# Kernel tuning notes

Hardware: AMD Instinct MI355X
Metric: run time of the kernel (lower is better)

## Reference

```python
import jax, jax.numpy as jnp
import numpy as np

H, D = 4, 64          # n_heads, feats_per_head (hidden_size = H*D = 256)
NEG_SLOPE = 0.2       # DGL GATv2Conv default negative_slope

N_GT, N_UBS, N_AG = 100000, 20000, 20000
E_SEEN, E_NEAR = 320000, 160000
F_GT, F_UBS, F_AG = 8, 8, 16
HID = H * D


def _linear_params(key, fan_in, fan_out):
    kw, kb = jax.random.split(key)
    s = 1.0 / np.sqrt(fan_in)
    W = jax.random.uniform(kw, (fan_in, fan_out), jnp.float32, -s, s)
    b = jax.random.uniform(kb, (fan_out,), jnp.float32, -s, s)
    return W, b


def setup_inputs() -> dict:
    key = jax.random.key(0)
    ks = jax.random.split(key, 16)
    inp = {
        'x_gt': jax.random.normal(ks[0], (N_GT, F_GT), jnp.float32),
        'x_ubs': jax.random.normal(ks[1], (N_UBS, F_UBS), jnp.float32),
        'x_agent': jax.random.normal(ks[2], (N_AG, F_AG), jnp.float32),
        'seen_src': jax.random.randint(ks[3], (E_SEEN,), 0, N_GT, jnp.int32),
        'seen_dst': jax.random.randint(ks[4], (E_SEEN,), 0, N_AG, jnp.int32),
        'near_src': jax.random.randint(ks[5], (E_NEAR,), 0, N_UBS, jnp.int32),
        'near_dst': jax.random.randint(ks[6], (E_NEAR,), 0, N_AG, jnp.int32),
    }
    # GATv2Conv 'seen': (gt -> agent)
    inp['Ws_seen'], inp['bs_seen'] = _linear_params(ks[7], F_GT, HID)
    inp['Wd_seen'], inp['bd_seen'] = _linear_params(ks[8], F_AG, HID)
    inp['attn_seen'] = jax.random.normal(ks[9], (H, D), jnp.float32) * 0.1
    inp['Wr_seen'], inp['br_seen'] = _linear_params(ks[10], F_AG, HID)
    # GATv2Conv 'near': (ubs -> agent)
    inp['Ws_near'], inp['bs_near'] = _linear_params(ks[11], F_UBS, HID)
    inp['Wd_near'], inp['bd_near'] = _linear_params(ks[12], F_AG, HID)
    inp['attn_near'] = jax.random.normal(ks[13], (H, D), jnp.float32) * 0.1
    inp['Wr_near'], inp['br_near'] = _linear_params(ks[14], F_AG, HID)
    # aggregation MLP: Linear(2*HID, HID) + ReLU
    inp['W_aggr'], inp['b_aggr'] = _linear_params(ks[15], 2 * HID, HID)
    return inp


def _gatv2(h_src, h_dst, src, dst, Ws, bs, Wd, bd, attn, Wr, br, n_dst):
    # DGL GATv2Conv, bipartite, residual=True, allow_zero_in_degree, ReLU activation
    fs = (h_src @ Ws + bs).reshape(-1, H, D)   # [Ns,H,D]
    fd = (h_dst @ Wd + bd).reshape(-1, H, D)   # [Nd,H,D]
    e = jax.nn.leaky_relu(fs[src] + fd[dst], NEG_SLOPE)     # [E,H,D]
    scores = jnp.einsum('ehd,hd->eh', e, attn)              # [E,H]
    # edge softmax over incoming edges of each dst node
    m = jax.ops.segment_max(scores, dst, num_segments=n_dst)
    m = jnp.where(jnp.isfinite(m), m, 0.0)                  # zero-in-degree guard
    ex = jnp.exp(scores - m[dst])
    denom = jax.ops.segment_sum(ex, dst, num_segments=n_dst)
    alpha = ex / denom[dst]                                 # [E,H]
    rst = jax.ops.segment_sum(alpha[:, :, None] * fs[src], dst, num_segments=n_dst)
    rst = rst + (h_dst @ Wr + br).reshape(-1, H, D)         # residual
    return jax.nn.relu(rst).reshape(n_dst, H * D)


def reference(x_gt, x_ubs, x_agent, seen_src, seen_dst, near_src, near_dst,
              Ws_seen, bs_seen, Wd_seen, bd_seen, attn_seen, Wr_seen, br_seen,
              Ws_near, bs_near, Wd_near, bd_near, attn_near, Wr_near, br_near,
              W_aggr, b_aggr):
    n_ag = x_agent.shape[0]
    x1 = _gatv2(x_gt, x_agent, seen_src, seen_dst,
                Ws_seen, bs_seen, Wd_seen, bd_seen, attn_seen, Wr_seen, br_seen, n_ag)
    x2 = _gatv2(x_ubs, x_agent, near_src, near_dst,
                Ws_near, bs_near, Wd_near, bd_near, attn_near, Wr_near, br_near, n_ag)
    x_out = jnp.concatenate((x1, x2), axis=1)               # [N_ag, 2*HID]
    return jax.nn.relu(x_out @ W_aggr + b_aggr)             # [N_ag, HID]
```

## Files before the change

kernel.cpp:

```cpp
#include <hip/hip_runtime.h>
#include <math.h>

#define NEG 0.2f
#define CAP 48

typedef short bf16x8 __attribute__((ext_vector_type(8)));
typedef float f32x4  __attribute__((ext_vector_type(4)));
typedef float f32x2  __attribute__((ext_vector_type(2)));

static __device__ __forceinline__ f32x2 pkfma(f32x2 a, f32x2 b, f32x2 c) {
    return __builtin_elementwise_fma(a, b, c);
}
static __device__ __forceinline__ f32x2 splat2(float x) { return (f32x2){x, x}; }

static __device__ __forceinline__ unsigned short f2bf(float f) {
    unsigned int x = __float_as_uint(f);
    unsigned int r = (x + 0x7FFFu + ((x >> 16) & 1u)) >> 16;
    return (unsigned short)r;
}
static __device__ __forceinline__ float rlane(float v, int l) {
    return __int_as_float(__builtin_amdgcn_readlane(__float_as_int(v), l));
}

#define DPP_ADD(x, ctrl) \
    ((x) + __int_as_float(__builtin_amdgcn_update_dpp( \
        __float_as_int(x), __float_as_int(x), (ctrl), 0xF, 0xF, true)))
static __device__ __forceinline__ float rowsum16(float v) {
    v = DPP_ADD(v, 0xB1);
    v = DPP_ADD(v, 0x4E);
    v = DPP_ADD(v, 0x141);
    v = DPP_ADD(v, 0x140);
    return v;
}

__global__ void k_hist_scatter(
    const int* __restrict__ src_s, const int* __restrict__ dst_s, int Es,
    const int* __restrict__ src_n, const int* __restrict__ dst_n, int En,
    int* __restrict__ deg_s, int* __restrict__ deg_n,
    int* __restrict__ csr_s, int* __restrict__ csr_n,
    const float* __restrict__ W, unsigned short* __restrict__ Wt)
{
    int i = blockIdx.x * 256 + threadIdx.x;
    if (i < Es) {
        int d = dst_s[i];
        int p = atomicAdd(&deg_s[d], 1);
        if (p < CAP) csr_s[d * CAP + p] = src_s[i];
    }
    int j = i - Es;
    if (j >= 0 && j < En) {
        int d = dst_n[j];
        int p = atomicAdd(&deg_n[d], 1);
        if (p < CAP) csr_n[d * CAP + p] = src_n[j];
    }
    if (i < 512 * 256) {
        int k = i >> 8, n = i & 255;
        Wt[(size_t)n * 512 + k] = f2bf(W[i]);
    }
}

#define EDGE_BODY { \
    f32x2 x0 = splat2(rlane(r0, j * 8 + 0)); \
    f32x2 x1 = splat2(rlane(r0, j * 8 + 1)); \
    f32x2 x2 = splat2(rlane(r0, j * 8 + 2)); \
    f32x2 x3 = splat2(rlane(r0, j * 8 + 3)); \
    f32x2 x4 = splat2(rlane(r0, j * 8 + 4)); \
    f32x2 x5 = splat2(rlane(r0, j * 8 + 5)); \
    f32x2 x6 = splat2(rlane(r0, j * 8 + 6)); \
    f32x2 x7 = splat2(rlane(r0, j * 8 + 7)); \
    f32x2 fs01 = bs01, fs23 = bs23; \
    fs01 = pkfma(x0, ws01[0], fs01); fs23 = pkfma(x0, ws23[0], fs23); \
    fs01 = pkfma(x1, ws01[1], fs01); fs23 = pkfma(x1, ws23[1], fs23); \
    fs01 = pkfma(x2, ws01[2], fs01); fs23 = pkfma(x2, ws23[2], fs23); \
    fs01 = pkfma(x3, ws01[3], fs01); fs23 = pkfma(x3, ws23[3], fs23); \
    fs01 = pkfma(x4, ws01[4], fs01); fs23 = pkfma(x4, ws23[4], fs23); \
    fs01 = pkfma(x5, ws01[5], fs01); fs23 = pkfma(x5, ws23[5], fs23); \
    fs01 = pkfma(x6, ws01[6], fs01); fs23 = pkfma(x6, ws23[6], fs23); \
    fs01 = pkfma(x7, ws01[7], fs01); fs23 = pkfma(x7, ws23[7], fs23); \
    f32x2 t01 = fs01 + fd01r; \
    f32x2 t23 = fs23 + fd23r; \
    t01 = __builtin_elementwise_max(t01, NEG * t01); \
    t23 = __builtin_elementwise_max(t23, NEG * t23); \
    f32x2 scp = t01 * at01; \
    scp = pkfma(t23, at23, scp); \
    float sc = scp.x + scp.y; \
    sc = rowsum16(sc); \
    float p = __expf(sc);    \
    l += p; \
    f32x2 pp = splat2(p); \
    a01 = pkfma(pp, fs01, a01); \
    a23 = pkfma(pp, fs23, a23); }

static __device__ __forceinline__ void gat_layer4(
    const float* __restrict__ x_src, const int* __restrict__ csr,
    const float* __restrict__ Ws, const float* __restrict__ bs,
    const float* __restrict__ Wd, const float* __restrict__ bd,
    const float* __restrict__ at,
    const float* __restrict__ Wr, const float* __restrict__ br,
    float xag, int lane, int wave, int nb, int n_dst,
    const int* st, const int* dg,
    const int* i1pre, const float* x0pre,
    unsigned short* __restrict__ xcat, int col)
{
    const int d0 = lane * 4;
    const int gs = lane >> 3;
    const int w8 = lane & 7;

    f32x2 fd01[4], fd23[4], fr01[4], fr23[4];
    {
        float4 bdv = *(const float4*)&bd[d0];
        float4 brv = *(const float4*)&br[d0];
#pragma unroll
        for (int j = 0; j < 4; ++j) {
            fd01[j] = (f32x2){bdv.x, bdv.y}; fd23[j] = (f32x2){bdv.z, bdv.w};
            fr01[j] = (f32x2){brv.x, brv.y}; fr23[j] = (f32x2){brv.z, brv.w};
        }
#pragma unroll
        for (int k = 0; k < 16; ++k) {
            float4 wd = *(const float4*)&Wd[k * 256 + d0];
            float4 wr = *(const float4*)&Wr[k * 256 + d0];
            f32x2 wd01 = {wd.x, wd.y}, wd23 = {wd.z, wd.w};
            f32x2 wr01 = {wr.x, wr.y}, wr23 = {wr.z, wr.w};
#pragma unroll
            for (int j = 0; j < 4; ++j) {
                f32x2 xk = splat2(rlane(xag, j * 16 + k));
                fd01[j] = pkfma(xk, wd01, fd01[j]);
                fd23[j] = pkfma(xk, wd23, fd23[j]);
                fr01[j] = pkfma(xk, wr01, fr01[j]);
                fr23[j] = pkfma(xk, wr23, fr23[j]);
            }
        }
    }

    f32x2 ws01[8], ws23[8];
#pragma unroll
    for (int k = 0; k < 8; ++k) {
        float4 w = *(const float4*)&Ws[k * 256 + d0];
        ws01[k] = (f32x2){w.x, w.y};
        ws23[k] = (f32x2){w.z, w.w};
    }
    f32x2 bs01, bs23, at01, at23;
    {
        float4 b4 = *(const float4*)&bs[d0];
        float4 a4 = *(const float4*)&at[d0];
        bs01 = (f32x2){b4.x, b4.y}; bs23 = (f32x2){b4.z, b4.w};
        at01 = (f32x2){a4.x, a4.y}; at23 = (f32x2){a4.z, a4.w};
    }

#pragma unroll
    for (int rep = 0; rep < 4; ++rep) {
        const int node = nb + rep * 4 + wave;
        if (node >= n_dst) continue;

        const int start = st[rep];
        const int deg   = dg[rep];
        const f32x2 fd01r = fd01[rep], fd23r = fd23[rep];

        float l = 0.f;
        f32x2 a01 = {0.f, 0.f}, a23 = {0.f, 0.f};

        if (deg > 0) {
            float r0 = x0pre[rep];
            int   i1 = i1pre[rep];
            const int nfull = deg >> 3, tail = deg & 7;

            for (int c = 0; c < nfull; ++c) {
                float r1 = x_src[(size_t)i1 * 8 + w8];
                int e2 = c * 8 + 16 + gs; e2 = (e2 < deg) ? e2 : deg - 1;
                int i2 = csr[start + e2];
#pragma unroll
                for (int j = 0; j < 8; ++j) EDGE_BODY
                r0 = r1; i1 = i2;
            }
            if (tail) {
#pragma unroll
                for (int j = 0; j < 8; ++j)
                    if (j < tail) EDGE_BODY
            }
        }

        float inv = (l > 0.f) ? 1.f / l : 0.f;
        ushort4 o;
        o.x = f2bf(fmaxf(fmaf(a01.x, inv, fr01[rep].x), 0.f));
        o.y = f2bf(fmaxf(fmaf(a01.y, inv, fr01[rep].y), 0.f));
        o.z = f2bf(fmaxf(fmaf(a23.x, inv, fr23[rep].x), 0.f));
        o.w = f2bf(fmaxf(fmaf(a23.y, inv, fr23[rep].y), 0.f));
        *(ushort4*)&xcat[(size_t)node * 512 + col + d0] = o;
    }
}

__global__ __launch_bounds__(256) void k_gat(
    const float* __restrict__ xsrc_s, const int* __restrict__ deg_s_a, const int* __restrict__ csr_s,
    const float* __restrict__ Ws_s, const float* __restrict__ bs_s,
    const float* __restrict__ Wd_s, const float* __restrict__ bd_s,
    const float* __restrict__ at_s,
    const float* __restrict__ Wr_s, const float* __restrict__ br_s,
    const float* __restrict__ xsrc_n, const int* __restrict__ deg_n_a, const int* __restrict__ csr_n,
    const float* __restrict__ Ws_n, const float* __restrict__ bs_n,
    const float* __restrict__ Wd_n, const float* __restrict__ bd_n,
    const float* __restrict__ at_n,
    const float* __restrict__ Wr_n, const float* __restrict__ br_n,
    const float* __restrict__ x_ag,
    unsigned short* __restrict__ xcat, int n_dst, int gNs)
{
    const bool seen = (int)blockIdx.x < gNs;
    const int blk = seen ? (int)blockIdx.x : (int)blockIdx.x - gNs;

    const float* x_src = seen ? xsrc_s : xsrc_n;
    const int*   degp  = seen ? deg_s_a : deg_n_a;
    const int*   csr   = seen ? csr_s  : csr_n;
    const float* Ws    = seen ? Ws_s   : Ws_n;
    const float* bs    = seen ? bs_s   : bs_n;
    const float* Wd    = seen ? Wd_s   : Wd_n;
    const float* bd    = seen ? bd_s   : bd_n;
    const float* at    = seen ? at_s   : at_n;
    const float* Wr    = seen ? Wr_s   : Wr_n;
    const float* br    = seen ? br_s   : br_n;
    const int col = seen ? 0 : 256;

    const int t = threadIdx.x;
    const int wave = t >> 6, lane = t & 63;
    const int gs = lane >> 3, w8 = lane & 7;
    const int nb = blk * 16;

    int gnode = nb + ((lane >> 4) << 2) + wave;
    int gn = (gnode < n_dst) ? gnode : (n_dst - 1);
    float xag = x_ag[(size_t)gn * 16 + (lane & 15)];

    int st[4], dg[4];
#pragma unroll
    for (int j = 0; j < 4; ++j) {
        int nd = nb + j * 4 + wave;
        nd = (nd < n_dst) ? nd : (n_dst - 1);
        int d = degp[nd];
        dg[j] = (d < CAP) ? d : CAP;
        st[j] = nd * CAP;
    }

    int i0[4], i1[4];
#pragma unroll
    for (int j = 0; j < 4; ++j) {
        int dgj = dg[j];
        if (dgj > 0) {
            int e0 = (gs < dgj) ? gs : dgj - 1;
            int e1 = (8 + gs < dgj) ? 8 + gs : dgj - 1;
            i0[j] = csr[st[j] + e0];
            i1[j] = csr[st[j] + e1];
        } else { i0[j] = 0; i1[j] = 0; }
    }
    float x0[4];
#pragma unroll
    for (int j = 0; j < 4; ++j)
        x0[j] = x_src[(size_t)i0[j] * 8 + w8];

    gat_layer4(x_src, csr, Ws, bs, Wd, bd, at, Wr, br,
               xag, lane, wave, nb, n_dst, st, dg, i1, x0, xcat, col);
}

__global__ __launch_bounds__(256) void k_mlp(
    const unsigned short* __restrict__ X, const unsigned short* __restrict__ Wt,
    const float* __restrict__ b, float* __restrict__ out, int M)
{
    const int t = threadIdx.x;
    const int wave = t >> 6, lane = t & 63;
    const int m16 = lane & 15, q = lane >> 4;
    const int rbase = blockIdx.x * 16;
    const int nbase = wave * 64;

    int rowa = rbase + m16; if (rowa >= M) rowa = M - 1;
    const unsigned short* xp = X + (size_t)rowa * 512 + q * 8;
    const unsigned short* w0 = Wt + (size_t)(nbase + m16) * 512 + q * 8;
    const unsigned short* w1 = w0 + 16 * 512;
    const unsigned short* w2 = w0 + 32 * 512;
    const unsigned short* w3 = w0 + 48 * 512;

    f32x4 ac0 = {0.f, 0.f, 0.f, 0.f}, ac1 = ac0, ac2 = ac0, ac3 = ac0;

#pragma unroll
    for (int k0 = 0; k0 < 512; k0 += 32) {
        bf16x8 a  = *(const bf16x8*)(xp + k0);
        bf16x8 b0 = *(const bf16x8*)(w0 + k0);
        bf16x8 b1 = *(const bf16x8*)(w1 + k0);
        bf16x8 b2 = *(const bf16x8*)(w2 + k0);
        bf16x8 b3 = *(const bf16x8*)(w3 + k0);
        ac0 = __builtin_amdgcn_mfma_f32_16x16x32_bf16(a, b0, ac0, 0, 0, 0);
        ac1 = __builtin_amdgcn_mfma_f32_16x16x32_bf16(a, b1, ac1, 0, 0, 0);
        ac2 = __builtin_amdgcn_mfma_f32_16x16x32_bf16(a, b2, ac2, 0, 0, 0);
        ac3 = __builtin_amdgcn_mfma_f32_16x16x32_bf16(a, b3, ac3, 0, 0, 0);
    }

#define EPI(AC, J) { \
        int coln = nbase + (J) * 16 + m16; \
        float bias = b[coln]; \
        _Pragma("unroll") \
        for (int r = 0; r < 4; ++r) { \
            int orow = rbase + q * 4 + r; \
            if (orow < M) \
                out[(size_t)orow * 256 + coln] = fmaxf(AC[r] + bias, 0.f); \
        } }
    EPI(ac0, 0) EPI(ac1, 1) EPI(ac2, 2) EPI(ac3, 3)
#undef EPI
}

extern "C" void kernel_launch(void* const* d_in, const int* in_sizes, int n_in,
                              void* d_out, int out_size, void* d_ws, size_t ws_size,
                              hipStream_t stream) {
    const float* x_gt   = (const float*)d_in[0];
    const float* x_ubs  = (const float*)d_in[1];
    const float* x_ag   = (const float*)d_in[2];
    const int* seen_src = (const int*)d_in[3];
    const int* seen_dst = (const int*)d_in[4];
    const int* near_src = (const int*)d_in[5];
    const int* near_dst = (const int*)d_in[6];
    const float* Ws_s = (const float*)d_in[7];  const float* bs_s = (const float*)d_in[8];
    const float* Wd_s = (const float*)d_in[9];  const float* bd_s = (const float*)d_in[10];
    const float* at_s = (const float*)d_in[11];
    const float* Wr_s = (const float*)d_in[12]; const float* br_s = (const float*)d_in[13];
    const float* Ws_n = (const float*)d_in[14]; const float* bs_n = (const float*)d_in[15];
    const float* Wd_n = (const float*)d_in[16]; const float* bd_n = (const float*)d_in[17];
    const float* at_n = (const float*)d_in[18];
    const float* Wr_n = (const float*)d_in[19]; const float* br_n = (const float*)d_in[20];
    const float* W_a  = (const float*)d_in[21]; const float* b_a  = (const float*)d_in[22];

    const int n_ag = in_sizes[2] / 16;
    const int E_s  = in_sizes[3];
    const int E_n  = in_sizes[5];
    const int gN   = (n_ag + 15) / 16;

    char* ws = (char*)d_ws;
    int* deg_s = (int*)ws;              ws += (size_t)n_ag * 4;
    int* deg_n = (int*)ws;              ws += (size_t)n_ag * 4;
    int* csr_s = (int*)ws;              ws += (size_t)n_ag * CAP * 4;
    int* csr_n = (int*)ws;              ws += (size_t)n_ag * CAP * 4;
    unsigned short* xcat = (unsigned short*)ws;  ws += (size_t)n_ag * 512 * 2;
    unsigned short* Wt   = (unsigned short*)ws;

    hipMemsetAsync(deg_s, 0, (size_t)n_ag * 8, stream);

    int gE = (E_s + E_n + 255) / 256;
    k_hist_scatter<<<gE, 256, 0, stream>>>(
        seen_src, seen_dst, E_s, near_src, near_dst, E_n,
        deg_s, deg_n, csr_s, csr_n, W_a, Wt);

    k_gat<<<2 * gN, 256, 0, stream>>>(
        x_gt,  deg_s, csr_s, Ws_s, bs_s, Wd_s, bd_s, at_s, Wr_s, br_s,
        x_ubs, deg_n, csr_n, Ws_n, bs_n, Wd_n, bd_n, at_n, Wr_n, br_n,
        x_ag, xcat, n_ag, gN);

    k_mlp<<<gN, 256, 0, stream>>>(xcat, Wt, b_a, (float*)d_out, n_ag);
}
```

Measured before the change: 258.2 us.

## Fuse aggregation MLP into GAT kernel via per-tile completion counter

Merges the final MLP kernel into the GAT kernel. Each 16-row tile is written by two blocks, one for 'seen' and one for 'near'; each increments an atomic counter, and the second block to finish runs the MFMA MLP for that tile. This removes one kernel launch and lets the MLP for finished tiles overlap with GAT work on other tiles. In exchange it adds threadfence and atomic overhead, and the MLP work falls unevenly on whichever block finishes last.

```diff
diff --git a/kernel.cpp b/kernel.cpp
--- a/kernel.cpp
+++ b/kernel.cpp
@@ -188,7 +188,7 @@
     }
 }
 
-__global__ __launch_bounds__(256) void k_gat(
+__global__ __launch_bounds__(256) void k_gatmlp(
     const float* __restrict__ xsrc_s, const int* __restrict__ deg_s_a, const int* __restrict__ csr_s,
     const float* __restrict__ Ws_s, const float* __restrict__ bs_s,
     const float* __restrict__ Wd_s, const float* __restrict__ bd_s,
@@ -200,7 +200,9 @@
     const float* __restrict__ at_n,
     const float* __restrict__ Wr_n, const float* __restrict__ br_n,
     const float* __restrict__ x_ag,
-    unsigned short* __restrict__ xcat, int n_dst, int gNs)
+    const unsigned short* __restrict__ Wt, const float* __restrict__ bmlp,
+    int* __restrict__ done, unsigned short* __restrict__ xcat,
+    float* __restrict__ out, int n_dst, int gNs)
 {
     const bool seen = (int)blockIdx.x < gNs;
     const int blk = seen ? (int)blockIdx.x : (int)blockIdx.x - gNs;
@@ -254,27 +256,27 @@
 
     gat_layer4(x_src, csr, Ws, bs, Wd, bd, at, Wr, br,
                xag, lane, wave, nb, n_dst, st, dg, i1, x0, xcat, col);
-}
-
-__global__ __launch_bounds__(256) void k_mlp(
-    const unsigned short* __restrict__ X, const unsigned short* __restrict__ Wt,
-    const float* __restrict__ b, float* __restrict__ out, int M)
-{
-    const int t = threadIdx.x;
-    const int wave = t >> 6, lane = t & 63;
+
+    __syncthreads();
+    __shared__ int sh_old;
+    if (t == 0) {
+        __threadfence();
+        sh_old = atomicAdd(&done[blk], 1);
+    }
+    __syncthreads();
+    if (sh_old != 1) return;
+    __threadfence();
+
     const int m16 = lane & 15, q = lane >> 4;
-    const int rbase = blockIdx.x * 16;
     const int nbase = wave * 64;
-
-    int rowa = rbase + m16; if (rowa >= M) rowa = M - 1;
-    const unsigned short* xp = X + (size_t)rowa * 512 + q * 8;
+    int rowa = nb + m16; if (rowa >= n_dst) rowa = n_dst - 1;
+    const unsigned short* xp = xcat + (size_t)rowa * 512 + q * 8;
     const unsigned short* w0 = Wt + (size_t)(nbase + m16) * 512 + q * 8;
     const unsigned short* w1 = w0 + 16 * 512;
     const unsigned short* w2 = w0 + 32 * 512;
     const unsigned short* w3 = w0 + 48 * 512;
 
     f32x4 ac0 = {0.f, 0.f, 0.f, 0.f}, ac1 = ac0, ac2 = ac0, ac3 = ac0;
-
 #pragma unroll
     for (int k0 = 0; k0 < 512; k0 += 32) {
         bf16x8 a  = *(const bf16x8*)(xp + k0);
@@ -290,12 +292,12 @@
 
 #define EPI(AC, J) { \
         int coln = nbase + (J) * 16 + m16; \
-        float bias = b[coln]; \
+        float bv = bmlp[coln]; \
         _Pragma("unroll") \
         for (int r = 0; r < 4; ++r) { \
-            int orow = rbase + q * 4 + r; \
-            if (orow < M) \
-                out[(size_t)orow * 256 + coln] = fmaxf(AC[r] + bias, 0.f); \
+            int orow = nb + q * 4 + r; \
+            if (orow < n_dst) \
+                out[(size_t)orow * 256 + coln] = fmaxf(AC[r] + bv, 0.f); \
         } }
     EPI(ac0, 0) EPI(ac1, 1) EPI(ac2, 2) EPI(ac3, 3)
 #undef EPI
@@ -329,22 +331,21 @@
     char* ws = (char*)d_ws;
     int* deg_s = (int*)ws;              ws += (size_t)n_ag * 4;
     int* deg_n = (int*)ws;              ws += (size_t)n_ag * 4;
+    int* done  = (int*)ws;              ws += (size_t)gN * 4;
     int* csr_s = (int*)ws;              ws += (size_t)n_ag * CAP * 4;
     int* csr_n = (int*)ws;              ws += (size_t)n_ag * CAP * 4;
     unsigned short* xcat = (unsigned short*)ws;  ws += (size_t)n_ag * 512 * 2;
     unsigned short* Wt   = (unsigned short*)ws;
 
-    hipMemsetAsync(deg_s, 0, (size_t)n_ag * 8, stream);
+    hipMemsetAsync(deg_s, 0, (size_t)n_ag * 8 + (size_t)gN * 4, stream);
 
     int gE = (E_s + E_n + 255) / 256;
     k_hist_scatter<<<gE, 256, 0, stream>>>(
         seen_src, seen_dst, E_s, near_src, near_dst, E_n,
         deg_s, deg_n, csr_s, csr_n, W_a, Wt);
 
-    k_gat<<<2 * gN, 256, 0, stream>>>(
+    k_gatmlp<<<2 * gN, 256, 0, stream>>>(
         x_gt,  deg_s, csr_s, Ws_s, bs_s, Wd_s, bd_s, at_s, Wr_s, br_s,
         x_ubs, deg_n, csr_n, Ws_n, bs_n, Wd_n, bd_n, at_n, Wr_n, br_n,
-        x_ag, xcat, n_ag, gN);
-
-    k_mlp<<<gN, 256, 0, stream>>>(xcat, Wt, b_a, (float*)d_out, n_ag);
-}
+        x_ag, Wt, b_a, done, xcat, (float*)d_out, n_ag, gN);
+}
```

After: 430.9 us. 1.67x slower.

## Make GAT kernel persistent with per-wave atomic work stealing over node groups

Applied to the files above, without the earlier changes.

Replaces the static grid over 16-node blocks with a persistent grid of 1024 blocks in which each wave repeatedly claims a 4-node item from a global atomic counter. Each wave now handles 4 consecutive destination nodes instead of nodes strided by wave index. The aim is better load balance across uneven in-degrees and less tail imbalance. The cost is an atomic per item, and because gat_layer4 is now called inside the loop, the Ws/Wd/Wr weight loads and the small projection are recomputed for every item. The counter is zeroed by extending the existing memset.

```diff
diff --git a/kernel.cpp b/kernel.cpp
--- a/kernel.cpp
+++ b/kernel.cpp
@@ -96,7 +96,7 @@
     const float* __restrict__ Wd, const float* __restrict__ bd,
     const float* __restrict__ at,
     const float* __restrict__ Wr, const float* __restrict__ br,
-    float xag, int lane, int wave, int nb, int n_dst,
+    float xag, int lane, int nodebase, int n_dst,
     const int* st, const int* dg,
     const int* i1pre, const float* x0pre,
     unsigned short* __restrict__ xcat, int col)
@@ -148,7 +148,7 @@
 
 #pragma unroll
     for (int rep = 0; rep < 4; ++rep) {
-        const int node = nb + rep * 4 + wave;
+        const int node = nodebase + rep;
         if (node >= n_dst) continue;
 
         const int start = st[rep];
@@ -200,60 +200,66 @@
     const float* __restrict__ at_n,
     const float* __restrict__ Wr_n, const float* __restrict__ br_n,
     const float* __restrict__ x_ag,
-    unsigned short* __restrict__ xcat, int n_dst, int gNs)
+    unsigned short* __restrict__ xcat, int* __restrict__ ctr,
+    int n_dst, int items_s, int items_total)
 {
-    const bool seen = (int)blockIdx.x < gNs;
-    const int blk = seen ? (int)blockIdx.x : (int)blockIdx.x - gNs;
-
-    const float* x_src = seen ? xsrc_s : xsrc_n;
-    const int*   degp  = seen ? deg_s_a : deg_n_a;
-    const int*   csr   = seen ? csr_s  : csr_n;
-    const float* Ws    = seen ? Ws_s   : Ws_n;
-    const float* bs    = seen ? bs_s   : bs_n;
-    const float* Wd    = seen ? Wd_s   : Wd_n;
-    const float* bd    = seen ? bd_s   : bd_n;
-    const float* at    = seen ? at_s   : at_n;
-    const float* Wr    = seen ? Wr_s   : Wr_n;
-    const float* br    = seen ? br_s   : br_n;
-    const int col = seen ? 0 : 256;
-
-    const int t = threadIdx.x;
-    const int wave = t >> 6, lane = t & 63;
+    const int lane = threadIdx.x & 63;
     const int gs = lane >> 3, w8 = lane & 7;
-    const int nb = blk * 16;
-
-    int gnode = nb + ((lane >> 4) << 2) + wave;
-    int gn = (gnode < n_dst) ? gnode : (n_dst - 1);
-    float xag = x_ag[(size_t)gn * 16 + (lane & 15)];
-
-    int st[4], dg[4];
-#pragma unroll
-    for (int j = 0; j < 4; ++j) {
-        int nd = nb + j * 4 + wave;
-        nd = (nd < n_dst) ? nd : (n_dst - 1);
-        int d = degp[nd];
-        dg[j] = (d < CAP) ? d : CAP;
-        st[j] = nd * CAP;
-    }
-
-    int i0[4], i1[4];
-#pragma unroll
-    for (int j = 0; j < 4; ++j) {
-        int dgj = dg[j];
-        if (dgj > 0) {
-            int e0 = (gs < dgj) ? gs : dgj - 1;
-            int e1 = (8 + gs < dgj) ? 8 + gs : dgj - 1;
-            i0[j] = csr[st[j] + e0];
-            i1[j] = csr[st[j] + e1];
-        } else { i0[j] = 0; i1[j] = 0; }
-    }
-    float x0[4];
-#pragma unroll
-    for (int j = 0; j < 4; ++j)
-        x0[j] = x_src[(size_t)i0[j] * 8 + w8];
-
-    gat_layer4(x_src, csr, Ws, bs, Wd, bd, at, Wr, br,
-               xag, lane, wave, nb, n_dst, st, dg, i1, x0, xcat, col);
+
+    for (;;) {
+        int id;
+        if (lane == 0) id = atomicAdd(ctr, 1);
+        id = __shfl(id, 0);
+        if (id >= items_total) return;
+
+        const bool seen = id < items_s;
+        const int nodebase = (seen ? id : id - items_s) * 4;
+
+        const float* x_src = seen ? xsrc_s : xsrc_n;
+        const int*   degp  = seen ? deg_s_a : deg_n_a;
+        const int*   csr   = seen ? csr_s  : csr_n;
+        const float* Ws    = seen ? Ws_s   : Ws_n;
+        const float* bs    = seen ? bs_s   : bs_n;
+        const float* Wd    = seen ? Wd_s   : Wd_n;
+        const float* bd    = seen ? bd_s   : bd_n;
+        const float* at    = seen ? at_s   : at_n;
+        const float* Wr    = seen ? Wr_s   : Wr_n;
+        const float* br    = seen ? br_s   : br_n;
+        const int col = seen ? 0 : 256;
+
+        int gnode = nodebase + (lane >> 4);
+        int gn = (gnode < n_dst) ? gnode : (n_dst - 1);
+        float xag = x_ag[(size_t)gn * 16 + (lane & 15)];
+
+        int st[4], dg[4];
+#pragma unroll
+        for (int j = 0; j < 4; ++j) {
+            int nd = nodebase + j;
+            nd = (nd < n_dst) ? nd : (n_dst - 1);
+            int d = degp[nd];
+            dg[j] = (d < CAP) ? d : CAP;
+            st[j] = nd * CAP;
+        }
+
+        int i0[4], i1[4];
+#pragma unroll
+        for (int j = 0; j < 4; ++j) {
+            int dgj = dg[j];
+            if (dgj > 0) {
+                int e0 = (gs < dgj) ? gs : dgj - 1;
+                int e1 = (8 + gs < dgj) ? 8 + gs : dgj - 1;
+                i0[j] = csr[st[j] + e0];
+                i1[j] = csr[st[j] + e1];
+            } else { i0[j] = 0; i1[j] = 0; }
+        }
+        float x0[4];
+#pragma unroll
+        for (int j = 0; j < 4; ++j)
+            x0[j] = x_src[(size_t)i0[j] * 8 + w8];
+
+        gat_layer4(x_src, csr, Ws, bs, Wd, bd, at, Wr, br,
+                   xag, lane, nodebase, n_dst, st, dg, i1, x0, xcat, col);
+    }
 }
 
 __global__ __launch_bounds__(256) void k_mlp(
@@ -325,26 +331,29 @@
     const int E_s  = in_sizes[3];
     const int E_n  = in_sizes[5];
     const int gN   = (n_ag + 15) / 16;
+    const int items_s = (n_ag + 3) / 4;
+    const int items_total = 2 * items_s;
 
     char* ws = (char*)d_ws;
     int* deg_s = (int*)ws;              ws += (size_t)n_ag * 4;
     int* deg_n = (int*)ws;              ws += (size_t)n_ag * 4;
+    int* ctr   = (int*)ws;              ws += 4;
     int* csr_s = (int*)ws;              ws += (size_t)n_ag * CAP * 4;
     int* csr_n = (int*)ws;              ws += (size_t)n_ag * CAP * 4;
     unsigned short* xcat = (unsigned short*)ws;  ws += (size_t)n_ag * 512 * 2;
     unsigned short* Wt   = (unsigned short*)ws;
 
-    hipMemsetAsync(deg_s, 0, (size_t)n_ag * 8, stream);
+    hipMemsetAsync(deg_s, 0, (size_t)n_ag * 8 + 4, stream);
 
     int gE = (E_s + E_n + 255) / 256;
     k_hist_scatter<<<gE, 256, 0, stream>>>(
         seen_src, seen_dst, E_s, near_src, near_dst, E_n,
         deg_s, deg_n, csr_s, csr_n, W_a, Wt);
 
-    k_gat<<<2 * gN, 256, 0, stream>>>(
+    k_gat<<<1024, 256, 0, stream>>>(
         x_gt,  deg_s, csr_s, Ws_s, bs_s, Wd_s, bd_s, at_s, Wr_s, br_s,
         x_ubs, deg_n, csr_n, Ws_n, bs_n, Wd_n, bd_n, at_n, Wr_n, br_n,
-        x_ag, xcat, n_ag, gN);
+        x_ag, xcat, ctr, n_ag, items_s, items_total);
 
     k_mlp<<<gN, 256, 0, stream>>>(xcat, Wt, b_a, (float*)d_out, n_ag);
 }
```

New measurement: 375.7 us. 1.46x slower.
